# Kernel optimization log

Measured on AMD Instinct MI355X. Metric: run time of the kernel, lower is better.

The kernel has to match this reference:

```python
import jax, jax.numpy as jnp
import numpy as np

B, S, E, D = 256, 256, 2, 128  # batch, seq_len, encoder_dim, decoder_dim


def setup_inputs() -> dict:
    key = jax.random.key(0)
    ks = jax.random.split(key, 9)
    u = lambda k, shape, n: jax.random.uniform(k, shape, jnp.float32, -1.0 / np.sqrt(n), 1.0 / np.sqrt(n))
    return {
        "out_encoder": jax.random.normal(ks[0], (B, S, E), jnp.float32),
        "W1_w": u(ks[1], (S, S), S),            # Linear(seq_len, seq_len)
        "W1_b": u(ks[2], (S,), S),
        "W2_w": u(ks[3], (S, 2 * S), 2 * S),    # Linear(2*seq_len, seq_len)
        "W2_b": u(ks[4], (S,), 2 * S),
        "W_ih": u(ks[5], (4 * D, E), D),        # LSTMCell input weights (i,f,g,o)
        "W_hh": u(ks[6], (4 * D, D), D),
        "b_ih": u(ks[7], (4 * D,), D),
        "b_hh": u(ks[8], (4 * D,), D),
    }


def reference(out_encoder, W1_w, W1_b, W2_w, W2_b, W_ih, W_hh, b_ih, b_hh):
    b, s, e = out_encoder.shape
    d = W_hh.shape[1]
    dt = out_encoder.dtype

    # W_2 term: encoder flattened to [B, 2S]; identical every step, hoist it.
    w2term = out_encoder.reshape(b, s * e) @ W2_w.T + W2_b          # [B, S]
    # W_1 applied to a row of S copies of h_d equals h_d * rowsum(W1) + b.
    w1sum = W1_w.sum(axis=1)                                        # [S]

    def attn(h):  # h: [B, D] -> context [B, E]
        hterm = h[:, :, None] * w1sum[None, None, :] + W1_b         # [B, D, S]
        en = jnp.tanh(w2term[:, None, :] + hterm)                   # [B, D, S]
        alpha = jax.nn.softmax(en, axis=-1).mean(axis=1)            # [B, S] (softmax over seq)
        return jnp.einsum('bs,bse->be', alpha, out_encoder)         # [B, E]

    def lstm_cell(x, h, c):
        gates = x @ W_ih.T + h @ W_hh.T + b_ih + b_hh               # [B, 4D]
        i, f, g, o = jnp.split(gates, 4, axis=-1)
        c = jax.nn.sigmoid(f) * c + jax.nn.sigmoid(i) * jnp.tanh(g)
        h = jax.nn.sigmoid(o) * jnp.tanh(c)
        return h, c

    h0 = jnp.zeros((b, d), dt)
    c0 = jnp.zeros((b, d), dt)

    def step(carry, _):
        h, c = carry
        x = attn(h)
        h, c = lstm_cell(x, h, c)
        return (h, c), h

    _, hs = jax.lax.scan(step, (h0, c0), None, length=s)
    return hs  # [S, B, D]: stacked decoder hidden states (original returns a list of h_t)
```

## Files before the change

kernel.cpp:

```cpp
#include <hip/hip_runtime.h>

#define NB 256
#define NS 256
#define NE 2
#define ND 128
#define NT 512
#define NN 16

typedef float vf4 __attribute__((ext_vector_type(4)));
typedef _Float16 f16x8 __attribute__((ext_vector_type(8)));
typedef _Float16 f16x2 __attribute__((ext_vector_type(2)));
typedef float f32x4 __attribute__((ext_vector_type(4)));

constexpr float L2E = 1.4426950408889634f;
constexpr float PI_F = 3.14159265358979323846f;

__device__ const float CT[16][16] = {
 {1,0,0,0,0,0,0,0,0,0,0,0,0,0,0,0},
 {0,1,0,0,0,0,0,0,0,0,0,0,0,0,0,0},
 {-1,0,2,0,0,0,0,0,0,0,0,0,0,0,0,0},
 {0,-3,0,4,0,0,0,0,0,0,0,0,0,0,0,0},
 {1,0,-8,0,8,0,0,0,0,0,0,0,0,0,0,0},
 {0,5,0,-20,0,16,0,0,0,0,0,0,0,0,0,0},
 {-1,0,18,0,-48,0,32,0,0,0,0,0,0,0,0,0},
 {0,-7,0,56,0,-112,0,64,0,0,0,0,0,0,0,0},
 {1,0,-32,0,160,0,-256,0,128,0,0,0,0,0,0,0},
 {0,9,0,-120,0,432,0,-576,0,256,0,0,0,0,0},
 {-1,0,50,0,-400,0,1120,0,-1280,0,512,0,0,0,0,0},
 {0,-11,0,220,0,-1232,0,2816,0,-2816,0,1024,0,0,0,0},
 {1,0,-72,0,840,0,-3584,0,6912,0,-6144,0,2048,0,0,0},
 {0,13,0,-364,0,2912,0,-9984,0,16640,0,-13312,0,4096,0,0},
 {-1,0,98,0,-1568,0,9408,0,-26880,0,39424,0,-28672,0,8192,0},
 {0,-15,0,560,0,-6048,0,28800,0,-70400,0,92160,0,-61440,0,16384}};

template <int C>
__device__ __forceinline__ float dppadd(float x) {
    return x + __builtin_bit_cast(float,
        __builtin_amdgcn_update_dpp(0, __builtin_bit_cast(int, x), C, 0xF, 0xF, true));
}
__device__ __forceinline__ float red_wave64(float x) {
    x = dppadd<0xB1>(x); x = dppadd<0x4E>(x); x = dppadd<0x141>(x);
    x = dppadd<0x140>(x); x = dppadd<0x142>(x); x = dppadd<0x143>(x); return x;
}
__device__ __forceinline__ float red_half32(float x) {
    x = dppadd<0xB1>(x); x = dppadd<0x4E>(x); x = dppadd<0x141>(x);
    x = dppadd<0x140>(x); x = dppadd<0x142>(x); return x;
}
__device__ __forceinline__ float red16_all(float x) {
    x = dppadd<0xB1>(x);
    x = dppadd<0x4E>(x);
    x = dppadd<0x141>(x);
    x = dppadd<0x140>(x);
    return x;
}

__global__ __launch_bounds__(NT, 2)
void attn_lstm_decoder(const float* __restrict__ enc,
                       const float* __restrict__ W1w,
                       const float* __restrict__ W1b,
                       const float* __restrict__ W2w,
                       const float* __restrict__ W2b,
                       const float* __restrict__ Wih,
                       const float* __restrict__ Whh,
                       const float* __restrict__ bih,
                       const float* __restrict__ bhh,
                       float* __restrict__ out)
{
    const int b    = blockIdx.x;
    const int t    = threadIdx.x;
    const int wave = t >> 6;
    const int lane = t & 63;
    const int grp  = lane >> 4;
    const int nib  = lane & 15;
    const int gl   = 16 * wave + nib;
    const int half = lane >> 5;
    const int idx  = lane & 31;
    const int jnode = 2 * wave + half;

    __shared__ __align__(16) _Float16 hist16[2 * ND];
    __shared__ float A2_l[NS];
    __shared__ float g2_l[NS];
    __shared__ float e0_l[NS];
    __shared__ float e1_l[NS];
    __shared__ float Ml[NN * NN];
    __shared__ float2 Pn[NN];
    __shared__ float2 Vl[NN];
    __shared__ float Pm0[NN], Pm1[NN];

    {
        float v = enc[b * (NS * NE) + t];
        if (t & 1) e1_l[t >> 1] = v; else e0_l[t >> 1] = v;
    }
    if (t < NN * NN) {
        const int mi = t >> 4, mj = t & 15;
        const float w = (mi == 0) ? (1.0f / NN) : (2.0f / NN);
        Ml[t] = w * __cosf((float)(mi * (2 * mj + 1)) * (PI_F / (2 * NN)));
    }
    __syncthreads();

    for (int r = 0; r < 32; ++r) {
        const int s = wave * 32 + r;
        float p = W1w[s * NS + lane]       + W1w[s * NS + lane + 64]
                + W1w[s * NS + lane + 128] + W1w[s * NS + lane + 192];
        p = red_wave64(p);
        if (lane == 63) g2_l[s] = p * (2.0f * L2E);
        float qq = 0.0f;
        #pragma unroll
        for (int kk = 0; kk < 8; ++kk) {
            const int c = lane + kk * 64;
            const float ev = (c & 1) ? e1_l[c >> 1] : e0_l[c >> 1];
            qq = fmaf(ev, W2w[s * (2 * NS) + c], qq);
        }
        qq = red_wave64(qq);
        if (lane == 63) A2_l[s] = (qq + W2b[s] + W1b[s]) * (2.0f * L2E);
    }
    __syncthreads();

    {
        const float y  = __cosf((float)(2 * jnode + 1) * (PI_F / (2 * NN)));
        const float C2 = -2.0f * L2E;
        float l = 0.0f, p0 = 0.0f, p1 = 0.0f;
        #pragma unroll
        for (int k = 0; k < 8; ++k) {
            const int s = k * 32 + idx;
            const float m1 = fmaf(y, g2_l[s], A2_l[s]);
            const float u  = __builtin_amdgcn_exp2f(m1);
            const float rc = __builtin_amdgcn_rcpf(u + 1.0f);
            const float e  = __builtin_amdgcn_exp2f(rc * C2);
            l += e;
            p0 = fmaf(e, e0_l[s], p0);
            p1 = fmaf(e, e1_l[s], p1);
        }
        l = red_half32(l); p0 = red_half32(p0); p1 = red_half32(p1);
        if ((lane & 31) == 31) {
            const float rl = __builtin_amdgcn_rcpf(l);
            Pn[jnode] = make_float2(p0 * rl, p1 * rl);
        }
    }
    __syncthreads();

    if (t < NN) {
        float v0 = 0.0f, v1 = 0.0f;
        #pragma unroll
        for (int j = 0; j < NN; ++j) {
            v0 = fmaf(Ml[t * NN + j], Pn[j].x, v0);
            v1 = fmaf(Ml[t * NN + j], Pn[j].y, v1);
        }
        Vl[t] = make_float2(v0 * (1.0f / ND), v1 * (1.0f / ND));
    }

    f16x8 wf[4][4];
    #pragma unroll
    for (int rt = 0; rt < 4; ++rt) {
        const int row = 128 * rt + 16 * wave + nib;
        #pragma unroll
        for (int kt = 0; kt < 4; ++kt) {
            const vf4 wa = *reinterpret_cast<const vf4*>(Whh + row * ND + 32 * kt + 8 * grp);
            const vf4 wb = *reinterpret_cast<const vf4*>(Whh + row * ND + 32 * kt + 8 * grp + 4);
            f16x8 wv;
            wv[0] = (_Float16)wa.x; wv[1] = (_Float16)wa.y;
            wv[2] = (_Float16)wa.z; wv[3] = (_Float16)wa.w;
            wv[4] = (_Float16)wb.x; wv[5] = (_Float16)wb.y;
            wv[6] = (_Float16)wb.z; wv[7] = (_Float16)wb.w;
            wf[rt][kt] = wv;
        }
    }
    float wi0_[4], wi1_[4], bb_[4];
    #pragma unroll
    for (int j = 0; j < 4; ++j) {
        const int r = 128 * j + gl;
        wi0_[j] = Wih[r * 2 + 0];
        wi1_[j] = Wih[r * 2 + 1];
        bb_[j]  = bih[r] + bhh[r];
    }

    if (t < ND) hist16[ND + t] = (_Float16)0.0f;
    float h_reg = 0.0f, c_reg = 0.0f;
    __syncthreads();

    if (t < NN) {
        float s0 = 0.0f, s1 = 0.0f;
        #pragma unroll
        for (int k = 0; k < NN; ++k) {
            s0 = fmaf(Vl[k].x, CT[k][t], s0);
            s1 = fmaf(Vl[k].y, CT[k][t], s1);
        }
        Pm0[t] = s0; Pm1[t] = s1;
    }
    __syncthreads();

    float C0[16], C1[16];
    #pragma unroll
    for (int i = 0; i < 16; ++i) { C0[i] = Pm0[i]; C1[i] = Pm1[i]; }

    auto evalG = [&](float h, const float (&C)[16]) -> float {
        const float h2 = h * h;
        float e = C[14], o = C[15];
        #pragma unroll
        for (int k = 12; k >= 0; k -= 2) {
            e = fmaf(e, h2, C[k]);
            o = fmaf(o, h2, C[k + 1]);
        }
        return fmaf(h, o, e);
    };

    const int jpair = 32 * (nib >> 2) + 8 * grp + 2 * (nib & 3);
    const int idx16 = ((lane ^ 16) << 2);
    const int idx32 = ((lane ^ 32) << 2);

    for (int step = 0; step < NS; ++step) {
        const int rs = (step & 1) ^ 1;
        const int ws = step & 1;
        const _Float16* hb = &hist16[rs * ND];

        const f16x8 af0 = __builtin_bit_cast(f16x8, *reinterpret_cast<const int4*>(hb + 0  + 8 * grp));
        const f16x8 af1 = __builtin_bit_cast(f16x8, *reinterpret_cast<const int4*>(hb + 32 + 8 * grp));
        const f16x8 af2 = __builtin_bit_cast(f16x8, *reinterpret_cast<const int4*>(hb + 64 + 8 * grp));
        const f16x8 af3 = __builtin_bit_cast(f16x8, *reinterpret_cast<const int4*>(hb + 96 + 8 * grp));
        const f16x2 hp2 = *reinterpret_cast<const f16x2*>(hb + jpair);

        const float ha = (float)hp2[0];
        const float hc = (float)hp2[1];
        float r0 = evalG(ha, C0) + evalG(hc, C0);
        float r1 = evalG(ha, C1) + evalG(hc, C1);
        r0 = red16_all(r0); r1 = red16_all(r1);
        r0 += __builtin_bit_cast(float, __builtin_amdgcn_ds_bpermute(idx16, __builtin_bit_cast(int, r0)));
        r1 += __builtin_bit_cast(float, __builtin_amdgcn_ds_bpermute(idx16, __builtin_bit_cast(int, r1)));
        r0 += __builtin_bit_cast(float, __builtin_amdgcn_ds_bpermute(idx32, __builtin_bit_cast(int, r0)));
        r1 += __builtin_bit_cast(float, __builtin_amdgcn_ds_bpermute(idx32, __builtin_bit_cast(int, r1)));
        const float x0 = r0, x1 = r1;

        float ga[4];
        #pragma unroll
        for (int rt = 0; rt < 4; ++rt) {
            f32x4 a = {0.0f, 0.0f, 0.0f, 0.0f};
            a = __builtin_amdgcn_mfma_f32_16x16x32_f16(af0, wf[rt][0], a, 0, 0, 0);
            a = __builtin_amdgcn_mfma_f32_16x16x32_f16(af1, wf[rt][1], a, 0, 0, 0);
            a = __builtin_amdgcn_mfma_f32_16x16x32_f16(af2, wf[rt][2], a, 0, 0, 0);
            a = __builtin_amdgcn_mfma_f32_16x16x32_f16(af3, wf[rt][3], a, 0, 0, 0);
            ga[rt] = a[0];
        }

        const float gi = ga[0] + fmaf(x0, wi0_[0], fmaf(x1, wi1_[0], bb_[0]));
        const float gf = ga[1] + fmaf(x0, wi0_[1], fmaf(x1, wi1_[1], bb_[1]));
        const float gg = ga[2] + fmaf(x0, wi0_[2], fmaf(x1, wi1_[2], bb_[2]));
        const float go = ga[3] + fmaf(x0, wi0_[3], fmaf(x1, wi1_[3], bb_[3]));

        const float si = __builtin_amdgcn_rcpf(1.0f + __builtin_amdgcn_exp2f(-L2E * gi));
        const float sf = __builtin_amdgcn_rcpf(1.0f + __builtin_amdgcn_exp2f(-L2E * gf));
        const float so = __builtin_amdgcn_rcpf(1.0f + __builtin_amdgcn_exp2f(-L2E * go));
        const float tg = 1.0f - 2.0f * __builtin_amdgcn_rcpf(
            __builtin_amdgcn_exp2f(2.0f * L2E * gg) + 1.0f);
        c_reg = fmaf(sf, c_reg, si * tg);
        const float tc2 = 1.0f - 2.0f * __builtin_amdgcn_rcpf(
            __builtin_amdgcn_exp2f(2.0f * L2E * c_reg) + 1.0f);
        h_reg = so * tc2;

        if (grp == 0) {
            hist16[ws * ND + gl] = (_Float16)h_reg;
            out[(size_t)step * (NB * ND) + b * ND + gl] = h_reg;
        }

        asm volatile("s_waitcnt lgkmcnt(0)" ::: "memory");
        __builtin_amdgcn_s_barrier();
    }
}

extern "C" void kernel_launch(void* const* d_in, const int* in_sizes, int n_in,
                              void* d_out, int out_size, void* d_ws, size_t ws_size,
                              hipStream_t stream) {
    const float* enc = (const float*)d_in[0];
    const float* W1w = (const float*)d_in[1];
    const float* W1b = (const float*)d_in[2];
    const float* W2w = (const float*)d_in[3];
    const float* W2b = (const float*)d_in[4];
    const float* Wih = (const float*)d_in[5];
    const float* Whh = (const float*)d_in[6];
    const float* bih = (const float*)d_in[7];
    const float* bhh = (const float*)d_in[8];
    attn_lstm_decoder<<<NB, NT, 0, stream>>>(enc, W1w, W1b, W2w, W2b,
                                             Wih, Whh, bih, bhh, (float*)d_out);
}
```

Before: 312.1 us.

## Batch 16 sequences per block so recurrent MFMA uses full N dimension

Each block now processes 16 batch rows instead of one, so the 16x16x32 MFMA for the recurrent h@W_hh uses all 16 columns rather than wasting 15 of them. The grid drops from 256 blocks to 16. The Chebyshev attention polynomial is now evaluated right after h is produced, and its partial sums are exchanged through a shared buffer for the next step, which replaces the per-step cross-lane reductions. The risk is that only 16 blocks run on a GPU with many more CUs, and the prologue (W2 matvec, per-node softmax loop) becomes much more serial per thread.

```diff
diff --git a/kernel.cpp b/kernel.cpp
--- a/kernel.cpp
+++ b/kernel.cpp
@@ -4,12 +4,15 @@
 #define NS 256
 #define NE 2
 #define ND 128
+#define NBB 16
 #define NT 512
 #define NN 16
+#define SLOTH 136
+#define XSLOT 36
 
 typedef float vf4 __attribute__((ext_vector_type(4)));
 typedef _Float16 f16x8 __attribute__((ext_vector_type(8)));
-typedef _Float16 f16x2 __attribute__((ext_vector_type(2)));
+typedef _Float16 f16x4 __attribute__((ext_vector_type(4)));
 typedef float f32x4 __attribute__((ext_vector_type(4)));
 
 constexpr float L2E = 1.4426950408889634f;
@@ -42,17 +45,6 @@
     x = dppadd<0xB1>(x); x = dppadd<0x4E>(x); x = dppadd<0x141>(x);
     x = dppadd<0x140>(x); x = dppadd<0x142>(x); x = dppadd<0x143>(x); return x;
 }
-__device__ __forceinline__ float red_half32(float x) {
-    x = dppadd<0xB1>(x); x = dppadd<0x4E>(x); x = dppadd<0x141>(x);
-    x = dppadd<0x140>(x); x = dppadd<0x142>(x); return x;
-}
-__device__ __forceinline__ float red16_all(float x) {
-    x = dppadd<0xB1>(x);
-    x = dppadd<0x4E>(x);
-    x = dppadd<0x141>(x);
-    x = dppadd<0x140>(x);
-    return x;
-}
 
 __global__ __launch_bounds__(NT, 2)
 void attn_lstm_decoder(const float* __restrict__ enc,
@@ -66,30 +58,29 @@
                        const float* __restrict__ bhh,
                        float* __restrict__ out)
 {
-    const int b    = blockIdx.x;
+    const int b0   = blockIdx.x * NBB;
     const int t    = threadIdx.x;
     const int wave = t >> 6;
     const int lane = t & 63;
     const int grp  = lane >> 4;
     const int nib  = lane & 15;
-    const int gl   = 16 * wave + nib;
-    const int half = lane >> 5;
-    const int idx  = lane & 31;
-    const int jnode = 2 * wave + half;
-
-    __shared__ __align__(16) _Float16 hist16[2 * ND];
-    __shared__ float A2_l[NS];
+    const int chb  = 16 * wave + 4 * grp;
+
+    __shared__ __align__(16) _Float16 hist16[2 * NBB * SLOTH];
+    __shared__ __align__(16) float    xp[2 * NBB * XSLOT];
+    __shared__ float e0_l[NBB * NS];
+    __shared__ float e1_l[NBB * NS];
+    __shared__ float A2_l[NBB * NS];
     __shared__ float g2_l[NS];
-    __shared__ float e0_l[NS];
-    __shared__ float e1_l[NS];
     __shared__ float Ml[NN * NN];
-    __shared__ float2 Pn[NN];
-    __shared__ float2 Vl[NN];
-    __shared__ float Pm0[NN], Pm1[NN];
-
-    {
-        float v = enc[b * (NS * NE) + t];
-        if (t & 1) e1_l[t >> 1] = v; else e0_l[t >> 1] = v;
+    __shared__ float2 Pn2[NN * NBB];
+    __shared__ float2 Vl2[NN * NBB];
+    __shared__ float Pm0[NBB * NN], Pm1[NBB * NN];
+
+    #pragma unroll
+    for (int bi = 0; bi < NBB; ++bi) {
+        float v = enc[(size_t)(b0 + bi) * (NS * NE) + t];
+        if (t & 1) e1_l[bi * NS + (t >> 1)] = v; else e0_l[bi * NS + (t >> 1)] = v;
     }
     if (t < NN * NN) {
         const int mi = t >> 4, mj = t & 15;
@@ -104,55 +95,73 @@
                 + W1w[s * NS + lane + 128] + W1w[s * NS + lane + 192];
         p = red_wave64(p);
         if (lane == 63) g2_l[s] = p * (2.0f * L2E);
-        float qq = 0.0f;
-        #pragma unroll
-        for (int kk = 0; kk < 8; ++kk) {
-            const int c = lane + kk * 64;
-            const float ev = (c & 1) ? e1_l[c >> 1] : e0_l[c >> 1];
-            qq = fmaf(ev, W2w[s * (2 * NS) + c], qq);
-        }
-        qq = red_wave64(qq);
-        if (lane == 63) A2_l[s] = (qq + W2b[s] + W1b[s]) * (2.0f * L2E);
-    }
-    __syncthreads();
+    }
 
     {
-        const float y  = __cosf((float)(2 * jnode + 1) * (PI_F / (2 * NN)));
+        const int bi = t >> 5;
+        const int si = t & 31;
+        for (int r = 0; r < 8; ++r) {
+            const int s = si + 32 * r;
+            const vf4* w4 = reinterpret_cast<const vf4*>(W2w + (size_t)s * (2 * NS));
+            float qq = 0.0f;
+            for (int c4 = 0; c4 < NS / 2; ++c4) {
+                const vf4 wv = w4[c4];
+                qq = fmaf(e0_l[bi * NS + 2 * c4],     wv.x, qq);
+                qq = fmaf(e1_l[bi * NS + 2 * c4],     wv.y, qq);
+                qq = fmaf(e0_l[bi * NS + 2 * c4 + 1], wv.z, qq);
+                qq = fmaf(e1_l[bi * NS + 2 * c4 + 1], wv.w, qq);
+            }
+            A2_l[bi * NS + s] = (qq + W2b[s] + W1b[s]) * (2.0f * L2E);
+        }
+    }
+    __syncthreads();
+
+    if (t < NN * NBB) {
+        const int jn = t >> 4, bi = t & 15;
+        const float y  = __cosf((float)(2 * jn + 1) * (PI_F / (2 * NN)));
         const float C2 = -2.0f * L2E;
         float l = 0.0f, p0 = 0.0f, p1 = 0.0f;
-        #pragma unroll
-        for (int k = 0; k < 8; ++k) {
-            const int s = k * 32 + idx;
-            const float m1 = fmaf(y, g2_l[s], A2_l[s]);
+        for (int s = 0; s < NS; ++s) {
+            const float m1 = fmaf(y, g2_l[s], A2_l[bi * NS + s]);
             const float u  = __builtin_amdgcn_exp2f(m1);
             const float rc = __builtin_amdgcn_rcpf(u + 1.0f);
             const float e  = __builtin_amdgcn_exp2f(rc * C2);
             l += e;
-            p0 = fmaf(e, e0_l[s], p0);
-            p1 = fmaf(e, e1_l[s], p1);
-        }
-        l = red_half32(l); p0 = red_half32(p0); p1 = red_half32(p1);
-        if ((lane & 31) == 31) {
-            const float rl = __builtin_amdgcn_rcpf(l);
-            Pn[jnode] = make_float2(p0 * rl, p1 * rl);
-        }
-    }
-    __syncthreads();
-
-    if (t < NN) {
+            p0 = fmaf(e, e0_l[bi * NS + s], p0);
+            p1 = fmaf(e, e1_l[bi * NS + s], p1);
+        }
+        const float rl = __builtin_amdgcn_rcpf(l);
+        Pn2[jn * NBB + bi] = make_float2(p0 * rl, p1 * rl);
+    }
+    __syncthreads();
+
+    if (t < NN * NBB) {
+        const int i = t >> 4, bi = t & 15;
         float v0 = 0.0f, v1 = 0.0f;
         #pragma unroll
         for (int j = 0; j < NN; ++j) {
-            v0 = fmaf(Ml[t * NN + j], Pn[j].x, v0);
-            v1 = fmaf(Ml[t * NN + j], Pn[j].y, v1);
-        }
-        Vl[t] = make_float2(v0 * (1.0f / ND), v1 * (1.0f / ND));
+            v0 = fmaf(Ml[i * NN + j], Pn2[j * NBB + bi].x, v0);
+            v1 = fmaf(Ml[i * NN + j], Pn2[j * NBB + bi].y, v1);
+        }
+        Vl2[i * NBB + bi] = make_float2(v0 * (1.0f / ND), v1 * (1.0f / ND));
+    }
+    __syncthreads();
+
+    if (t < NN * NBB) {
+        const int m = t >> 4, bi = t & 15;
+        float s0 = 0.0f, s1 = 0.0f;
+        #pragma unroll
+        for (int k = 0; k < NN; ++k) {
+            s0 = fmaf(Vl2[k * NBB + bi].x, CT[k][m], s0);
+            s1 = fmaf(Vl2[k * NBB + bi].y, CT[k][m], s1);
+        }
+        Pm0[bi * NN + m] = s0; Pm1[bi * NN + m] = s1;
     }
 
     f16x8 wf[4][4];
     #pragma unroll
-    for (int rt = 0; rt < 4; ++rt) {
-        const int row = 128 * rt + 16 * wave + nib;
+    for (int j = 0; j < 4; ++j) {
+        const int row = 128 * j + 16 * wave + nib;
         #pragma unroll
         for (int kt = 0; kt < 4; ++kt) {
             const vf4 wa = *reinterpret_cast<const vf4*>(Whh + row * ND + 32 * kt + 8 * grp);
@@ -162,103 +171,131 @@
             wv[2] = (_Float16)wa.z; wv[3] = (_Float16)wa.w;
             wv[4] = (_Float16)wb.x; wv[5] = (_Float16)wb.y;
             wv[6] = (_Float16)wb.z; wv[7] = (_Float16)wb.w;
-            wf[rt][kt] = wv;
-        }
-    }
-    float wi0_[4], wi1_[4], bb_[4];
+            wf[j][kt] = wv;
+        }
+    }
+    float wi0_[4][4], wi1_[4][4], bb_[4][4];
     #pragma unroll
     for (int j = 0; j < 4; ++j) {
-        const int r = 128 * j + gl;
-        wi0_[j] = Wih[r * 2 + 0];
-        wi1_[j] = Wih[r * 2 + 1];
-        bb_[j]  = bih[r] + bhh[r];
-    }
-
-    if (t < ND) hist16[ND + t] = (_Float16)0.0f;
-    float h_reg = 0.0f, c_reg = 0.0f;
-    __syncthreads();
-
-    if (t < NN) {
-        float s0 = 0.0f, s1 = 0.0f;
-        #pragma unroll
-        for (int k = 0; k < NN; ++k) {
-            s0 = fmaf(Vl[k].x, CT[k][t], s0);
-            s1 = fmaf(Vl[k].y, CT[k][t], s1);
-        }
-        Pm0[t] = s0; Pm1[t] = s1;
-    }
-    __syncthreads();
-
-    float C0[16], C1[16];
+        #pragma unroll
+        for (int jj = 0; jj < 4; ++jj) {
+            const int r = 128 * j + chb + jj;
+            wi0_[j][jj] = Wih[r * 2 + 0];
+            wi1_[j][jj] = Wih[r * 2 + 1];
+            bb_[j][jj]  = bih[r] + bhh[r];
+        }
+    }
+
+    for (int i = t; i < 2 * NBB * SLOTH; i += NT) hist16[i] = (_Float16)0.0f;
+    float c_[4] = {0.f, 0.f, 0.f, 0.f};
+    __syncthreads();
+
+    float cc0[16], cc1[16];
     #pragma unroll
-    for (int i = 0; i < 16; ++i) { C0[i] = Pm0[i]; C1[i] = Pm1[i]; }
-
-    auto evalG = [&](float h, const float (&C)[16]) -> float {
+    for (int m = 0; m < NN; ++m) {
+        cc0[m] = Pm0[nib * NN + m];
+        cc1[m] = Pm1[nib * NN + m];
+    }
+
+    auto evalG2 = [&](float h, float& a0, float& a1) {
         const float h2 = h * h;
-        float e = C[14], o = C[15];
+        float e0v = cc0[14], o0v = cc0[15];
+        float e1v = cc1[14], o1v = cc1[15];
         #pragma unroll
         for (int k = 12; k >= 0; k -= 2) {
-            e = fmaf(e, h2, C[k]);
-            o = fmaf(o, h2, C[k + 1]);
-        }
-        return fmaf(h, o, e);
+            e0v = fmaf(e0v, h2, cc0[k]);
+            o0v = fmaf(o0v, h2, cc0[k + 1]);
+            e1v = fmaf(e1v, h2, cc1[k]);
+            o1v = fmaf(o1v, h2, cc1[k + 1]);
+        }
+        a0 += fmaf(h, o0v, e0v);
+        a1 += fmaf(h, o1v, e1v);
     };
 
-    const int jpair = 32 * (nib >> 2) + 8 * grp + 2 * (nib & 3);
-    const int idx16 = ((lane ^ 16) << 2);
-    const int idx32 = ((lane ^ 32) << 2);
+    {
+        float p0 = 4.0f * cc0[0];
+        float p1 = 4.0f * cc1[0];
+        p0 += __builtin_bit_cast(float, __builtin_amdgcn_ds_swizzle(__builtin_bit_cast(int, p0), 0x401F));
+        p1 += __builtin_bit_cast(float, __builtin_amdgcn_ds_swizzle(__builtin_bit_cast(int, p1), 0x401F));
+        if (!(lane & 16)) {
+            float2* xw = reinterpret_cast<float2*>(&xp[(0 * NBB + nib) * XSLOT]);
+            xw[2 * wave + (lane >> 5)] = make_float2(p0, p1);
+        }
+    }
+    __syncthreads();
+
+    const size_t outbase = (size_t)(b0 + nib) * ND + chb;
 
     for (int step = 0; step < NS; ++step) {
-        const int rs = (step & 1) ^ 1;
-        const int ws = step & 1;
-        const _Float16* hb = &hist16[rs * ND];
-
-        const f16x8 af0 = __builtin_bit_cast(f16x8, *reinterpret_cast<const int4*>(hb + 0  + 8 * grp));
-        const f16x8 af1 = __builtin_bit_cast(f16x8, *reinterpret_cast<const int4*>(hb + 32 + 8 * grp));
-        const f16x8 af2 = __builtin_bit_cast(f16x8, *reinterpret_cast<const int4*>(hb + 64 + 8 * grp));
-        const f16x8 af3 = __builtin_bit_cast(f16x8, *reinterpret_cast<const int4*>(hb + 96 + 8 * grp));
-        const f16x2 hp2 = *reinterpret_cast<const f16x2*>(hb + jpair);
-
-        const float ha = (float)hp2[0];
-        const float hc = (float)hp2[1];
-        float r0 = evalG(ha, C0) + evalG(hc, C0);
-        float r1 = evalG(ha, C1) + evalG(hc, C1);
-        r0 = red16_all(r0); r1 = red16_all(r1);
-        r0 += __builtin_bit_cast(float, __builtin_amdgcn_ds_bpermute(idx16, __builtin_bit_cast(int, r0)));
-        r1 += __builtin_bit_cast(float, __builtin_amdgcn_ds_bpermute(idx16, __builtin_bit_cast(int, r1)));
-        r0 += __builtin_bit_cast(float, __builtin_amdgcn_ds_bpermute(idx32, __builtin_bit_cast(int, r0)));
-        r1 += __builtin_bit_cast(float, __builtin_amdgcn_ds_bpermute(idx32, __builtin_bit_cast(int, r1)));
-        const float x0 = r0, x1 = r1;
-
-        float ga[4];
-        #pragma unroll
-        for (int rt = 0; rt < 4; ++rt) {
+        const int pr = step & 1;
+        const _Float16* hb = &hist16[(pr ^ 1) * NBB * SLOTH];
+
+        const vf4* xr = reinterpret_cast<const vf4*>(&xp[(pr * NBB + nib) * XSLOT]);
+        f32x4 xs = xr[0] + xr[1];
+        xs += xr[2] + xr[3];
+        xs += xr[4] + xr[5];
+        xs += xr[6] + xr[7];
+        const float x0 = xs[0] + xs[2];
+        const float x1 = xs[1] + xs[3];
+
+        f16x8 hf[4];
+        #pragma unroll
+        for (int kt = 0; kt < 4; ++kt)
+            hf[kt] = __builtin_bit_cast(f16x8,
+                *reinterpret_cast<const int4*>(hb + nib * SLOTH + 32 * kt + 8 * grp));
+
+        f32x4 acc[4];
+        #pragma unroll
+        for (int j = 0; j < 4; ++j) {
             f32x4 a = {0.0f, 0.0f, 0.0f, 0.0f};
-            a = __builtin_amdgcn_mfma_f32_16x16x32_f16(af0, wf[rt][0], a, 0, 0, 0);
-            a = __builtin_amdgcn_mfma_f32_16x16x32_f16(af1, wf[rt][1], a, 0, 0, 0);
-            a = __builtin_amdgcn_mfma_f32_16x16x32_f16(af2, wf[rt][2], a, 0, 0, 0);
-            a = __builtin_amdgcn_mfma_f32_16x16x32_f16(af3, wf[rt][3], a, 0, 0, 0);
-            ga[rt] = a[0];
-        }
-
-        const float gi = ga[0] + fmaf(x0, wi0_[0], fmaf(x1, wi1_[0], bb_[0]));
-        const float gf = ga[1] + fmaf(x0, wi0_[1], fmaf(x1, wi1_[1], bb_[1]));
-        const float gg = ga[2] + fmaf(x0, wi0_[2], fmaf(x1, wi1_[2], bb_[2]));
-        const float go = ga[3] + fmaf(x0, wi0_[3], fmaf(x1, wi1_[3], bb_[3]));
-
-        const float si = __builtin_amdgcn_rcpf(1.0f + __builtin_amdgcn_exp2f(-L2E * gi));
-        const float sf = __builtin_amdgcn_rcpf(1.0f + __builtin_amdgcn_exp2f(-L2E * gf));
-        const float so = __builtin_amdgcn_rcpf(1.0f + __builtin_amdgcn_exp2f(-L2E * go));
-        const float tg = 1.0f - 2.0f * __builtin_amdgcn_rcpf(
-            __builtin_amdgcn_exp2f(2.0f * L2E * gg) + 1.0f);
-        c_reg = fmaf(sf, c_reg, si * tg);
-        const float tc2 = 1.0f - 2.0f * __builtin_amdgcn_rcpf(
-            __builtin_amdgcn_exp2f(2.0f * L2E * c_reg) + 1.0f);
-        h_reg = so * tc2;
-
-        if (grp == 0) {
-            hist16[ws * ND + gl] = (_Float16)h_reg;
-            out[(size_t)step * (NB * ND) + b * ND + gl] = h_reg;
+            a = __builtin_amdgcn_mfma_f32_16x16x32_f16(wf[j][0], hf[0], a, 0, 0, 0);
+            a = __builtin_amdgcn_mfma_f32_16x16x32_f16(wf[j][1], hf[1], a, 0, 0, 0);
+            a = __builtin_amdgcn_mfma_f32_16x16x32_f16(wf[j][2], hf[2], a, 0, 0, 0);
+            a = __builtin_amdgcn_mfma_f32_16x16x32_f16(wf[j][3], hf[3], a, 0, 0, 0);
+            acc[j] = a;
+        }
+
+        float h_[4];
+        #pragma unroll
+        for (int jj = 0; jj < 4; ++jj) {
+            const float gi = acc[0][jj] + fmaf(x0, wi0_[0][jj], fmaf(x1, wi1_[0][jj], bb_[0][jj]));
+            const float gf = acc[1][jj] + fmaf(x0, wi0_[1][jj], fmaf(x1, wi1_[1][jj], bb_[1][jj]));
+            const float gg = acc[2][jj] + fmaf(x0, wi0_[2][jj], fmaf(x1, wi1_[2][jj], bb_[2][jj]));
+            const float go = acc[3][jj] + fmaf(x0, wi0_[3][jj], fmaf(x1, wi1_[3][jj], bb_[3][jj]));
+
+            const float si = __builtin_amdgcn_rcpf(1.0f + __builtin_amdgcn_exp2f(-L2E * gi));
+            const float sf = __builtin_amdgcn_rcpf(1.0f + __builtin_amdgcn_exp2f(-L2E * gf));
+            const float so = __builtin_amdgcn_rcpf(1.0f + __builtin_amdgcn_exp2f(-L2E * go));
+            const float tg = 1.0f - 2.0f * __builtin_amdgcn_rcpf(
+                __builtin_amdgcn_exp2f(2.0f * L2E * gg) + 1.0f);
+            c_[jj] = fmaf(sf, c_[jj], si * tg);
+            const float tc2 = 1.0f - 2.0f * __builtin_amdgcn_rcpf(
+                __builtin_amdgcn_exp2f(2.0f * L2E * c_[jj]) + 1.0f);
+            h_[jj] = so * tc2;
+        }
+
+        *reinterpret_cast<vf4*>(out + (size_t)step * (NB * ND) + outbase) =
+            *reinterpret_cast<const vf4*>(h_);
+
+        {
+            f16x4 hp;
+            hp[0] = (_Float16)h_[0]; hp[1] = (_Float16)h_[1];
+            hp[2] = (_Float16)h_[2]; hp[3] = (_Float16)h_[3];
+            *reinterpret_cast<f16x4*>(&hist16[(pr * NBB + nib) * SLOTH + chb]) = hp;
+        }
+
+        {
+            float p0 = 0.0f, p1 = 0.0f;
+            evalG2(h_[0], p0, p1);
+            evalG2(h_[1], p0, p1);
+            evalG2(h_[2], p0, p1);
+            evalG2(h_[3], p0, p1);
+            p0 += __builtin_bit_cast(float, __builtin_amdgcn_ds_swizzle(__builtin_bit_cast(int, p0), 0x401F));
+            p1 += __builtin_bit_cast(float, __builtin_amdgcn_ds_swizzle(__builtin_bit_cast(int, p1), 0x401F));
+            if (!(lane & 16)) {
+                float2* xw = reinterpret_cast<float2*>(&xp[((pr ^ 1) * NBB + nib) * XSLOT]);
+                xw[2 * wave + (lane >> 5)] = make_float2(p0, p1);
+            }
         }
 
         asm volatile("s_waitcnt lgkmcnt(0)" ::: "memory");
@@ -278,6 +315,6 @@
     const float* Whh = (const float*)d_in[6];
     const float* bih = (const float*)d_in[7];
     const float* bhh = (const float*)d_in[8];
-    attn_lstm_decoder<<<NB, NT, 0, stream>>>(enc, W1w, W1b, W2w, W2b,
-                                             Wih, Whh, bih, bhh, (float*)d_out);
+    attn_lstm_decoder<<<NB / NBB, NT, 0, stream>>>(enc, W1w, W1b, W2w, W2b,
+                                                   Wih, Whh, bih, bhh, (float*)d_out);
 }
```

Result: slower. 691.8 us (+121.7%).
